# Kernel optimization log

Measured on AMD Instinct MI355X. Metric: run time of the kernel, lower is better.

The kernel has to match this reference:

```python
import jax, jax.numpy as jnp
import numpy as np

H_IMG = 224
W_IMG = 224
CHUNK = 128   # triangles rasterized per scan step
EPS = 1e-8
N_VERTS = 6890
N_FACES = 13776
BATCH = 2


def setup_inputs() -> dict:
    key = jax.random.key(0)
    k0, k1, k2 = jax.random.split(key, 3)
    # vertices in front of the camera (z ~ 2.5) so triangles project into the image
    v = jax.random.normal(k0, (BATCH, N_VERTS, 3), jnp.float32) * 0.3 + jnp.array([0.0, 0.0, 2.5], jnp.float32)
    vc = jax.random.uniform(k1, (N_VERTS, 3), dtype=jnp.float32)          # per-vertex colors
    f = jax.random.randint(k2, (N_FACES, 3), 0, N_VERTS, dtype=jnp.int32)  # triangle list
    bgcolor = jnp.zeros((3,), jnp.float32)
    camera_f = jnp.array([500.0, 500.0], jnp.float32)
    camera_c = jnp.array([112.0, 112.0], jnp.float32)
    camera_t = jnp.zeros((3,), jnp.float32)
    camera_rt = jnp.zeros((3,), jnp.float32)
    return {"v": v, "vc": vc, "bgcolor": bgcolor, "camera_f": camera_f,
            "camera_c": camera_c, "camera_t": camera_t, "camera_rt": camera_rt, "f": f}


def _rodrigues(r):
    # axis-angle -> rotation matrix, safe at r = 0
    th = jnp.sqrt(jnp.sum(r * r) + 1e-12)
    k = r / th
    kx, ky, kz = k[0], k[1], k[2]
    z = jnp.zeros_like(kx)
    K = jnp.stack([jnp.stack([z, -kz, ky]),
                   jnp.stack([kz, z, -kx]),
                   jnp.stack([-ky, kx, z])])
    c, s = jnp.cos(th), jnp.sin(th)
    return c * jnp.eye(3, dtype=r.dtype) + (1.0 - c) * jnp.outer(k, k) + s * K


def _edge(ax, ay, bx, by, px, py):
    # signed area of (a, b, p) * 2
    return (bx - ax) * (py - ay) - (by - ay) * (px - ax)


def _rasterize(uv, zc, vc, faces, bgcolor, height, width):
    """Z-buffered rasterization with perspective-correct barycentric color interp.
    uv: [V,2] screen coords, zc: [V] camera-space depth, vc: [V,C], faces: [F,3]."""
    F, C = faces.shape[0], vc.shape[-1]
    pad = (-F) % CHUNK
    faces_p = jnp.concatenate([faces, jnp.zeros((pad, 3), faces.dtype)], 0)
    fmask = jnp.concatenate([jnp.ones((F,), bool), jnp.zeros((pad,), bool)])
    faces_p = faces_p.reshape(-1, CHUNK, 3)
    fmask = fmask.reshape(-1, CHUNK)

    xs = jnp.arange(width, dtype=jnp.float32) + 0.5
    ys = jnp.arange(height, dtype=jnp.float32) + 0.5
    px, py = jnp.meshgrid(xs, ys)              # [H,W] pixel centers
    cx = px.ravel()[None, :]                    # [1,HW]
    cy = py.ravel()[None, :]
    HW = height * width
    ar = jnp.arange(HW)

    def step(carry, inp):
        zbuf, col = carry
        fc, fm = inp                            # [K,3] int, [K] bool
        p = uv[fc]                              # [K,3,2]
        zt = zc[fc]                             # [K,3]
        x0, y0 = p[:, 0, 0:1], p[:, 0, 1:2]
        x1, y1 = p[:, 1, 0:1], p[:, 1, 1:2]
        x2, y2 = p[:, 2, 0:1], p[:, 2, 1:2]
        w0 = _edge(x1, y1, x2, y2, cx, cy)      # [K,HW]
        w1 = _edge(x2, y2, x0, y0, cx, cy)
        w2 = _edge(x0, y0, x1, y1, cx, cy)
        area = _edge(x0, y0, x1, y1, x2, y2)    # [K,1]
        nz = jnp.abs(area) > EPS
        inv_area = jnp.where(nz, 1.0 / jnp.where(nz, area, 1.0), 0.0)
        b0, b1, b2 = w0 * inv_area, w1 * inv_area, w2 * inv_area
        inside = (b0 >= 0) & (b1 >= 0) & (b2 >= 0)
        zvalid = jnp.all(zt > EPS, axis=1, keepdims=True)
        valid = inside & zvalid & nz & fm[:, None]
        zt_s = jnp.maximum(zt, EPS)
        inv_z = b0 / zt_s[:, 0:1] + b1 / zt_s[:, 1:2] + b2 / zt_s[:, 2:3]
        zp = jnp.where(valid & (inv_z > EPS), 1.0 / jnp.maximum(inv_z, EPS), jnp.inf)
        idx = jnp.argmin(zp, axis=0)            # nearest triangle per pixel in chunk
        zmin = zp[idx, ar]                      # [HW]
        hit = jnp.isfinite(zmin)
        zmin_s = jnp.where(hit, zmin, 1.0)
        bb = jnp.stack([b0, b1, b2], -1)[idx, ar]   # [HW,3]
        fsel = fc[idx]                          # [HW,3]
        zsel = jnp.maximum(zt[idx], EPS)        # [HW,3]
        csel = vc[fsel]                         # [HW,3,C]
        pc = bb / zsel                          # perspective-correct weights / z
        newcol = jnp.einsum('pk,pkc->pc', pc, csel) * zmin_s[:, None]
        upd = hit & (zmin < zbuf)
        zbuf = jnp.where(upd, zmin_s, zbuf)
        col = jnp.where(upd[:, None], newcol, col)
        return (zbuf, col), None

    zbuf0 = jnp.full((HW,), jnp.inf, jnp.float32)
    col0 = jnp.broadcast_to(bgcolor.astype(jnp.float32), (HW, C))
    (zbuf, col), _ = jax.lax.scan(step, (zbuf0, col0), (faces_p, fmask))
    return col.reshape(height, width, C)


def reference(v, vc, bgcolor, camera_f, camera_c, camera_t, camera_rt, f):
    R = _rodrigues(camera_rt)
    vcam = jnp.einsum('bvj,ij->bvi', v, R) + camera_t   # [B,V,3]
    z = vcam[..., 2]
    zs = jnp.maximum(z, EPS)
    uv = vcam[..., :2] / zs[..., None] * camera_f + camera_c  # pinhole projection
    render = jax.vmap(lambda uv_b, z_b: _rasterize(uv_b, z_b, vc, f, bgcolor, H_IMG, W_IMG))
    return render(uv, z)                                   # [B,H,W,C]
```

## Files before the change

kernel.cpp:

```cpp
#include <hip/hip_runtime.h>
#include <math.h>

#define H_IMG 224
#define W_IMG 224
#define HW (H_IMG * W_IMG)
#define EPSF 1e-8f
#define NV 6890
#define NF 13776
#define NB 2
#define FCHUNK 128
#define NCHUNK ((NF + FCHUNK - 1) / FCHUNK)
#define FPAD (NCHUNK * FCHUNK)
#define NWAVE 8
#define NBUCK 1024
#define CHDR_STRIDE 128
#define KEY_INIT 0x7F800000FFFFFFFFULL

#define OFF_ZBU   0u
#define OFF_ZBS   110336u
#define OFF_BBS   220928u
#define OFF_GMS   663296u
#define OFF_OIS   2432768u
#define OFF_INV   2543360u
#define OFF_CHDR  2653696u
#define OFF_CNT   2654720u
#define OFF_OFFS  2662912u

__device__ inline unsigned long long shfl_xor_u64(unsigned long long v, int m) {
  unsigned lo = (unsigned)v, hi = (unsigned)(v >> 32);
  lo = __shfl_xor(lo, m);
  hi = __shfl_xor(hi, m);
  return ((unsigned long long)hi << 32) | lo;
}

struct Cam { float m[9]; float t0, t1, t2, fx, fy, cx, cy; };

__device__ inline Cam load_cam(const float* cf, const float* cc,
                               const float* ct, const float* crt) {
  Cam C;
  float r0 = crt[0], r1 = crt[1], r2 = crt[2];
  float ss = __fadd_rn(__fadd_rn(__fmul_rn(r0, r0), __fmul_rn(r1, r1)), __fmul_rn(r2, r2));
  float th = sqrtf(__fadd_rn(ss, 1e-12f));
  float kx = r0 / th, ky = r1 / th, kz = r2 / th;
  float c = cosf(th), s = sinf(th), oc = 1.0f - c;
  C.m[0] = c + oc * kx * kx;      C.m[1] = oc * kx * ky - s * kz; C.m[2] = oc * kx * kz + s * ky;
  C.m[3] = oc * ky * kx + s * kz; C.m[4] = c + oc * ky * ky;      C.m[5] = oc * ky * kz - s * kx;
  C.m[6] = oc * kz * kx - s * ky; C.m[7] = oc * kz * ky + s * kx; C.m[8] = c + oc * kz * kz;
  C.t0 = ct[0]; C.t1 = ct[1]; C.t2 = ct[2];
  C.fx = cf[0]; C.fy = cf[1]; C.cx = cc[0]; C.cy = cc[1];
  return C;
}

__device__ inline float3 proj_one(const Cam& C, const float* vp) {
  float x = vp[0], y = vp[1], z = vp[2];
  float xc = C.m[0] * x + C.m[1] * y + C.m[2] * z + C.t0;
  float yc = C.m[3] * x + C.m[4] * y + C.m[5] * z + C.t1;
  float zc = C.m[6] * x + C.m[7] * y + C.m[8] * z + C.t2;
  float zs = fmaxf(zc, EPSF);
  float u = __fadd_rn(__fmul_rn(xc / zs, C.fx), C.cx);
  float w = __fadd_rn(__fmul_rn(yc / zs, C.fy), C.cy);
  return make_float3(u, w, zc);
}

__global__ void zb_init_kernel(const float* __restrict__ v, const int* __restrict__ f,
                               const float* __restrict__ cf, const float* __restrict__ cc,
                               const float* __restrict__ ct, const float* __restrict__ crt,
                               float* __restrict__ zbU, unsigned* __restrict__ cnt,
                               float* __restrict__ zbS, float4* __restrict__ bbS) {
  int i = blockIdx.x * blockDim.x + threadIdx.x;
  if (i < NB * FPAD) {
    zbS[i] = 3e30f;
    bbS[i] = make_float4(1e30f, -1e30f, 1e30f, -1e30f);
  }
  if (i >= NB * NF) return;
  int b = i / NF, fi = i - b * NF;
  Cam C = load_cam(cf, cc, ct, crt);
  int i0 = f[fi * 3 + 0], i1 = f[fi * 3 + 1], i2 = f[fi * 3 + 2];
  float3 p0 = proj_one(C, v + ((size_t)b * NV + i0) * 3);
  float3 p1 = proj_one(C, v + ((size_t)b * NV + i1) * 3);
  float3 p2 = proj_one(C, v + ((size_t)b * NV + i2) * 3);
  float area = __fsub_rn(__fmul_rn(__fsub_rn(p1.x, p0.x), __fsub_rn(p2.y, p0.y)),
                         __fmul_rn(__fsub_rn(p1.y, p0.y), __fsub_rn(p2.x, p0.x)));
  bool nz = fabsf(area) > EPSF;
  bool zv = (p0.z > EPSF) && (p1.z > EPSF) && (p2.z > EPSF);
  bool ok = nz && zv;
  float zb;
  if (!ok) {
    zb = 3e30f;
  } else {
    float minz = fminf(fminf(fmaxf(p0.z, EPSF), fmaxf(p1.z, EPSF)), fmaxf(p2.z, EPSF));
    float M = fmaxf(fmaxf(fmaxf(fabsf(p0.x), fabsf(p0.y)), fmaxf(fabsf(p1.x), fabsf(p1.y))),
                    fmaxf(fabsf(p2.x), fabsf(p2.y)));
    float werr = (2.0f * M) * (M + 256.0f) * 6e-7f;
    bool tight = (3.0f * werr) <= (5e-4f * fabsf(area));
    zb = tight ? __fmul_rn(minz, 0.999f) : 0.0f;
  }
  zbU[i] = zb;
  int bucket = (int)fminf(fmaxf(zb * 256.0f, 0.0f), (float)(NBUCK - 1));
  atomicAdd(&cnt[b * NBUCK + bucket], 1u);
}

__global__ __launch_bounds__(1024) void scan_kernel(const unsigned* __restrict__ cnt,
                                                    unsigned* __restrict__ offs,
                                                    unsigned* __restrict__ chdr) {
  __shared__ unsigned wsum[16];
  __shared__ unsigned ends[NBUCK];
  int t = threadIdx.x, b = blockIdx.x;
  int lane = t & 63, wid = t >> 6;
  unsigned v = cnt[b * NBUCK + t];
  unsigned acc = v;
  #pragma unroll
  for (int d = 1; d < 64; d <<= 1) {
    unsigned n = __shfl_up(acc, d);
    if (lane >= d) acc += n;
  }
  if (lane == 63) wsum[wid] = acc;
  __syncthreads();
  if (t < 16) {
    unsigned wv = wsum[t];
    #pragma unroll
    for (int d = 1; d < 16; d <<= 1) {
      unsigned n = __shfl_up(wv, d, 16);
      if (t >= d) wv += n;
    }
    wsum[t] = wv;
  }
  __syncthreads();
  unsigned base = (wid > 0) ? wsum[wid - 1] : 0u;
  unsigned incl = base + acc;
  offs[b * NBUCK + t] = incl - v;
  ends[t] = incl;
  __syncthreads();
  if (t < NCHUNK) {
    unsigned pos0 = (unsigned)(t * FCHUNK);
    int lo = 0, hi = NBUCK - 1;
    while (lo < hi) {
      int mid = (lo + hi) >> 1;
      if (ends[mid] > pos0) hi = mid; else lo = mid + 1;
    }
    chdr[b * CHDR_STRIDE + t] = __float_as_uint((float)lo * (1.0f / 256.0f));
  }
}

__global__ void scatter_kernel(const float* __restrict__ v, const int* __restrict__ f,
                               const float* __restrict__ cf, const float* __restrict__ cc,
                               const float* __restrict__ ct, const float* __restrict__ crt,
                               const float* __restrict__ zbU, unsigned* __restrict__ offs,
                               float* __restrict__ zbS, float4* __restrict__ bbS,
                               float4* __restrict__ gmS, int* __restrict__ oiS,
                               int* __restrict__ inv) {
  int i = blockIdx.x * blockDim.x + threadIdx.x;
  if (i >= NB * NF) return;
  int b = i / NF, fi = i - b * NF;
  float zb = zbU[i];
  int bucket = (int)fminf(fmaxf(zb * 256.0f, 0.0f), (float)(NBUCK - 1));
  unsigned pos = atomicAdd(&offs[b * NBUCK + bucket], 1u);
  Cam C = load_cam(cf, cc, ct, crt);
  int i0 = f[fi * 3 + 0], i1 = f[fi * 3 + 1], i2 = f[fi * 3 + 2];
  float3 p0 = proj_one(C, v + ((size_t)b * NV + i0) * 3);
  float3 p1 = proj_one(C, v + ((size_t)b * NV + i1) * 3);
  float3 p2 = proj_one(C, v + ((size_t)b * NV + i2) * 3);
  float x0 = p0.x, y0 = p0.y, z0 = p0.z;
  float x1 = p1.x, y1 = p1.y, z1 = p1.z;
  float x2 = p2.x, y2 = p2.y, z2 = p2.z;
  float area = __fsub_rn(__fmul_rn(__fsub_rn(x1, x0), __fsub_rn(y2, y0)),
                         __fmul_rn(__fsub_rn(y1, y0), __fsub_rn(x2, x0)));
  bool nz = fabsf(area) > EPSF;
  float inv_area = nz ? (1.0f / area) : 0.0f;
  bool zv = (z0 > EPSF) && (z1 > EPSF) && (z2 > EPSF);
  bool ok = nz && zv;
  float zz0 = ok ? fmaxf(z0, EPSF) : 1e30f;
  float zz1 = ok ? fmaxf(z1, EPSF) : 1e30f;
  float zz2 = ok ? fmaxf(z2, EPSF) : 1e30f;
  size_t sp_ = (size_t)b * FPAD + pos;
  zbS[sp_] = zb;
  bbS[sp_] = make_float4(fminf(fminf(x0, x1), x2), fmaxf(fmaxf(x0, x1), x2),
                         fminf(fminf(y0, y1), y2), fmaxf(fmaxf(y0, y1), y2));
  gmS[sp_ * 4 + 0] = make_float4(__fsub_rn(x2, x1), __fsub_rn(y2, y1), x1, y1);
  gmS[sp_ * 4 + 1] = make_float4(__fsub_rn(x0, x2), __fsub_rn(y0, y2), x2, y2);
  gmS[sp_ * 4 + 2] = make_float4(__fsub_rn(x1, x0), __fsub_rn(y1, y0), x0, y0);
  gmS[sp_ * 4 + 3] = make_float4(zz0, zz1, zz2, inv_area);
  oiS[sp_] = fi;
  inv[i] = (int)pos;
}

__global__ __launch_bounds__(512) void raster_kernel(
    const unsigned* __restrict__ chdr,
    const float* __restrict__ zbS,
    const float4* __restrict__ bbS,
    const float4* __restrict__ gmS,
    const int* __restrict__ oiS,
    const int* __restrict__ inv,
    const int* __restrict__ f,
    const float* __restrict__ vc,
    const float* __restrict__ bg,
    float* __restrict__ out) {
  __shared__ unsigned hint[NWAVE][16];
  __shared__ unsigned long long fin[NWAVE][16];
  int b = blockIdx.z;
  int w = threadIdx.x >> 6;
  int lane = threadIdx.x & 63;
  int slot = lane & 3;
  int p = lane >> 2;
  int wx = blockIdx.x * 4, wy = blockIdx.y * 4;
  int x = wx + (p & 3), y = wy + (p >> 2);
  float px = (float)x + 0.5f, py = (float)y + 0.5f;
  float tx0 = (float)wx + 0.5f, tx1 = (float)wx + 3.5f;
  float ty0 = (float)wy + 0.5f, ty1 = (float)wy + 3.5f;
  const unsigned* chdrB = chdr + b * CHDR_STRIDE;
  const float*  zbB = zbS + (size_t)b * FPAD;
  const float4* bbB = bbS + (size_t)b * FPAD;
  const float4* gmB = gmS + (size_t)b * FPAD * 4;
  const int*    oiB = oiS + (size_t)b * FPAD;

  if (threadIdx.x < NWAVE * 16) hint[threadIdx.x >> 4][threadIdx.x & 15] = 0x7F800000u;
  __syncthreads();

  unsigned long long bestKey = KEY_INIT;

  for (int c = w; c < NCHUNK; c += NWAVE) {
    unsigned z_ = (unsigned)(bestKey >> 32);
    unsigned zo = __shfl_xor(z_, 1); if (zo < z_) z_ = zo;
    zo = __shfl_xor(z_, 2); if (zo < z_) z_ = zo;
    if (slot == 0) hint[w][p] = z_;
    unsigned bzp = hint[0][p];
    #pragma unroll
    for (int hw_ = 1; hw_ < NWAVE; ++hw_) {
      unsigned hh = hint[hw_][p]; if (hh < bzp) bzp = hh;
    }
    float comb = __uint_as_float(bzp);
    float czb = __uint_as_float(chdrB[c]);
    if (!__any(czb <= comb)) break;
    float combMax = fmaxf(comb, __shfl_xor(comb, 4));
    combMax = fmaxf(combMax, __shfl_xor(combMax, 8));
    combMax = fmaxf(combMax, __shfl_xor(combMax, 16));
    combMax = fmaxf(combMax, __shfl_xor(combMax, 32));
    int base = c * FCHUNK;
    #pragma unroll
    for (int h = 0; h < FCHUNK / 64; ++h) {
      int fbase = base + h * 64;
      float zb_lane = zbB[fbase + lane];
      float4 bb = bbB[fbase + lane];
      bool pass = (zb_lane <= combMax) &&
                  (bb.x <= tx1) && (bb.y >= tx0) &&
                  (bb.z <= ty1) && (bb.w >= ty0);
      unsigned long long m = __ballot(pass);
      unsigned long long mm = m;
      while (mm) {
        int bit = __builtin_ctzll(mm);
        int g = bit & ~3;
        mm &= ~(0xFULL << g);
        if ((m >> (g + slot)) & 1) {
          int fi = fbase + g + slot;
          const float4* gm = &gmB[(size_t)fi * 4];
          float4 q0 = gm[0], q1 = gm[1], q2 = gm[2], q3 = gm[3];
          float w0 = __fsub_rn(__fmul_rn(q0.x, __fsub_rn(py, q0.w)),
                               __fmul_rn(q0.y, __fsub_rn(px, q0.z)));
          float w1 = __fsub_rn(__fmul_rn(q1.x, __fsub_rn(py, q1.w)),
                               __fmul_rn(q1.y, __fsub_rn(px, q1.z)));
          float w2 = __fsub_rn(__fmul_rn(q2.x, __fsub_rn(py, q2.w)),
                               __fmul_rn(q2.y, __fsub_rn(px, q2.z)));
          float b0 = __fmul_rn(w0, q3.w);
          float b1 = __fmul_rn(w1, q3.w);
          float b2 = __fmul_rn(w2, q3.w);
          if (b0 >= 0.0f && b1 >= 0.0f && b2 >= 0.0f) {
            float invz = __fadd_rn(__fadd_rn(b0 / q3.x, b1 / q3.y), b2 / q3.z);
            if (invz > EPSF) {
              float zp = 1.0f / invz;
              unsigned long long key =
                  ((unsigned long long)__float_as_uint(zp) << 32) | (unsigned)oiB[fi];
              if (key < bestKey) bestKey = key;
            }
          }
        }
      }
    }
  }

  unsigned long long o = shfl_xor_u64(bestKey, 1);
  if (o < bestKey) bestKey = o;
  o = shfl_xor_u64(bestKey, 2);
  if (o < bestKey) bestKey = o;
  if (slot == 0) fin[w][p] = bestKey;
  __syncthreads();

  int t = threadIdx.x;
  if (t < 16) {
    unsigned long long key = fin[0][t];
    #pragma unroll
    for (int hw_ = 1; hw_ < NWAVE; ++hw_) {
      unsigned long long kk = fin[hw_][t]; if (kk < key) key = kk;
    }
    int xx = wx + (t & 3), yy = wy + (t >> 2);
    float pxx = (float)xx + 0.5f, pyy = (float)yy + 0.5f;
    float o0, o1, o2;
    if (key != KEY_INIT) {
      int best = (int)(unsigned)(key & 0xFFFFFFFFu);
      float zmin = __uint_as_float((unsigned)(key >> 32));
      int pos = inv[b * NF + best];
      const float4* g = &gmB[(size_t)pos * 4];
      float4 q0 = g[0], q1 = g[1], q2 = g[2], q3 = g[3];
      float w0 = __fsub_rn(__fmul_rn(q0.x, __fsub_rn(pyy, q0.w)),
                           __fmul_rn(q0.y, __fsub_rn(pxx, q0.z)));
      float w1 = __fsub_rn(__fmul_rn(q1.x, __fsub_rn(pyy, q1.w)),
                           __fmul_rn(q1.y, __fsub_rn(pxx, q1.z)));
      float w2 = __fsub_rn(__fmul_rn(q2.x, __fsub_rn(pyy, q2.w)),
                           __fmul_rn(q2.y, __fsub_rn(pxx, q2.z)));
      float b0 = __fmul_rn(w0, q3.w), b1 = __fmul_rn(w1, q3.w), b2 = __fmul_rn(w2, q3.w);
      float pc0 = b0 / q3.x, pc1 = b1 / q3.y, pc2 = b2 / q3.z;
      int i0 = f[best * 3 + 0], i1 = f[best * 3 + 1], i2 = f[best * 3 + 2];
      const float* c0p = vc + (size_t)i0 * 3;
      const float* c1p = vc + (size_t)i1 * 3;
      const float* c2p = vc + (size_t)i2 * 3;
      o0 = __fmul_rn(__fadd_rn(__fadd_rn(__fmul_rn(pc0, c0p[0]), __fmul_rn(pc1, c1p[0])),
                               __fmul_rn(pc2, c2p[0])), zmin);
      o1 = __fmul_rn(__fadd_rn(__fadd_rn(__fmul_rn(pc0, c0p[1]), __fmul_rn(pc1, c1p[1])),
                               __fmul_rn(pc2, c2p[1])), zmin);
      o2 = __fmul_rn(__fadd_rn(__fadd_rn(__fmul_rn(pc0, c0p[2]), __fmul_rn(pc1, c1p[2])),
                               __fmul_rn(pc2, c2p[2])), zmin);
    } else {
      o0 = bg[0]; o1 = bg[1]; o2 = bg[2];
    }
    size_t oo = ((size_t)(b * H_IMG + yy) * W_IMG + xx) * 3;
    out[oo + 0] = o0;
    out[oo + 1] = o1;
    out[oo + 2] = o2;
  }
}

extern "C" void kernel_launch(void* const* d_in, const int* in_sizes, int n_in,
                              void* d_out, int out_size, void* d_ws, size_t ws_size,
                              hipStream_t stream) {
  const float* v   = (const float*)d_in[0];
  const float* vc  = (const float*)d_in[1];
  const float* bg  = (const float*)d_in[2];
  const float* cf  = (const float*)d_in[3];
  const float* cc  = (const float*)d_in[4];
  const float* ct  = (const float*)d_in[5];
  const float* crt = (const float*)d_in[6];
  const int*   f   = (const int*)d_in[7];
  float* out = (float*)d_out;
  char* ws = (char*)d_ws;

  float*    zbU   = (float*)(ws + OFF_ZBU);
  float*    zbS   = (float*)(ws + OFF_ZBS);
  float4*   bbS   = (float4*)(ws + OFF_BBS);
  float4*   gmS   = (float4*)(ws + OFF_GMS);
  int*      oiS   = (int*)(ws + OFF_OIS);
  int*      inv   = (int*)(ws + OFF_INV);
  unsigned* chdr  = (unsigned*)(ws + OFF_CHDR);
  unsigned* cnt   = (unsigned*)(ws + OFF_CNT);
  unsigned* offs  = (unsigned*)(ws + OFF_OFFS);

  hipMemsetAsync(cnt, 0, (size_t)NB * NBUCK * 4, stream);
  hipLaunchKernelGGL(zb_init_kernel, dim3((NB * FPAD + 255) / 256), dim3(256), 0, stream,
                     v, f, cf, cc, ct, crt, zbU, cnt, zbS, bbS);
  hipLaunchKernelGGL(scan_kernel, dim3(NB), dim3(1024), 0, stream, cnt, offs, chdr);
  hipLaunchKernelGGL(scatter_kernel, dim3((NB * NF + 255) / 256), dim3(256), 0, stream,
                     v, f, cf, cc, ct, crt, zbU, offs, zbS, bbS, gmS, oiS, inv);
  hipLaunchKernelGGL(raster_kernel, dim3(W_IMG / 4, H_IMG / 4, NB),
                     dim3(512), 0, stream,
                     chdr, zbS, bbS, gmS, oiS, inv, f, vc, bg, out);
}
```

Before: 339.2 us.

## Fuse preprocessing kernels into one cooperative kernel and halve raster waves per block

Result: no change. 335.6 us (-1.1%).

```diff
diff --git a/kernel.cpp b/kernel.cpp
--- a/kernel.cpp
+++ b/kernel.cpp
@@ -1,5 +1,8 @@
 #include <hip/hip_runtime.h>
+#include <hip/hip_cooperative_groups.h>
 #include <math.h>
+
+namespace cg = cooperative_groups;
 
 #define H_IMG 224
 #define W_IMG 224
@@ -11,7 +14,7 @@
 #define FCHUNK 128
 #define NCHUNK ((NF + FCHUNK - 1) / FCHUNK)
 #define FPAD (NCHUNK * FCHUNK)
-#define NWAVE 8
+#define NWAVE 4
 #define NBUCK 1024
 #define CHDR_STRIDE 128
 #define KEY_INIT 0x7F800000FFFFFFFFULL
@@ -62,129 +65,129 @@
   return make_float3(u, w, zc);
 }
 
-__global__ void zb_init_kernel(const float* __restrict__ v, const int* __restrict__ f,
-                               const float* __restrict__ cf, const float* __restrict__ cc,
-                               const float* __restrict__ ct, const float* __restrict__ crt,
-                               float* __restrict__ zbU, unsigned* __restrict__ cnt,
-                               float* __restrict__ zbS, float4* __restrict__ bbS) {
+__global__ void prep_kernel(const float* __restrict__ v, const int* __restrict__ f,
+                            const float* __restrict__ cf, const float* __restrict__ cc,
+                            const float* __restrict__ ct, const float* __restrict__ crt,
+                            float* __restrict__ zbU, unsigned* __restrict__ cnt,
+                            unsigned* __restrict__ offs, unsigned* __restrict__ chdr,
+                            float* __restrict__ zbS, float4* __restrict__ bbS,
+                            float4* __restrict__ gmS, int* __restrict__ oiS,
+                            int* __restrict__ inv) {
+  cg::grid_group grid = cg::this_grid();
   int i = blockIdx.x * blockDim.x + threadIdx.x;
+
+  if (i < NB * NBUCK) cnt[i] = 0u;
   if (i < NB * FPAD) {
     zbS[i] = 3e30f;
     bbS[i] = make_float4(1e30f, -1e30f, 1e30f, -1e30f);
   }
-  if (i >= NB * NF) return;
-  int b = i / NF, fi = i - b * NF;
-  Cam C = load_cam(cf, cc, ct, crt);
-  int i0 = f[fi * 3 + 0], i1 = f[fi * 3 + 1], i2 = f[fi * 3 + 2];
-  float3 p0 = proj_one(C, v + ((size_t)b * NV + i0) * 3);
-  float3 p1 = proj_one(C, v + ((size_t)b * NV + i1) * 3);
-  float3 p2 = proj_one(C, v + ((size_t)b * NV + i2) * 3);
-  float area = __fsub_rn(__fmul_rn(__fsub_rn(p1.x, p0.x), __fsub_rn(p2.y, p0.y)),
-                         __fmul_rn(__fsub_rn(p1.y, p0.y), __fsub_rn(p2.x, p0.x)));
-  bool nz = fabsf(area) > EPSF;
-  bool zv = (p0.z > EPSF) && (p1.z > EPSF) && (p2.z > EPSF);
-  bool ok = nz && zv;
-  float zb;
-  if (!ok) {
-    zb = 3e30f;
-  } else {
-    float minz = fminf(fminf(fmaxf(p0.z, EPSF), fmaxf(p1.z, EPSF)), fmaxf(p2.z, EPSF));
-    float M = fmaxf(fmaxf(fmaxf(fabsf(p0.x), fabsf(p0.y)), fmaxf(fabsf(p1.x), fabsf(p1.y))),
-                    fmaxf(fabsf(p2.x), fabsf(p2.y)));
-    float werr = (2.0f * M) * (M + 256.0f) * 6e-7f;
-    bool tight = (3.0f * werr) <= (5e-4f * fabsf(area));
-    zb = tight ? __fmul_rn(minz, 0.999f) : 0.0f;
-  }
-  zbU[i] = zb;
-  int bucket = (int)fminf(fmaxf(zb * 256.0f, 0.0f), (float)(NBUCK - 1));
-  atomicAdd(&cnt[b * NBUCK + bucket], 1u);
-}
-
-__global__ __launch_bounds__(1024) void scan_kernel(const unsigned* __restrict__ cnt,
-                                                    unsigned* __restrict__ offs,
-                                                    unsigned* __restrict__ chdr) {
-  __shared__ unsigned wsum[16];
+  grid.sync();
+
+  if (i < NB * NF) {
+    int b = i / NF, fi = i - b * NF;
+    Cam C = load_cam(cf, cc, ct, crt);
+    int i0 = f[fi * 3 + 0], i1 = f[fi * 3 + 1], i2 = f[fi * 3 + 2];
+    float3 p0 = proj_one(C, v + ((size_t)b * NV + i0) * 3);
+    float3 p1 = proj_one(C, v + ((size_t)b * NV + i1) * 3);
+    float3 p2 = proj_one(C, v + ((size_t)b * NV + i2) * 3);
+    float area = __fsub_rn(__fmul_rn(__fsub_rn(p1.x, p0.x), __fsub_rn(p2.y, p0.y)),
+                           __fmul_rn(__fsub_rn(p1.y, p0.y), __fsub_rn(p2.x, p0.x)));
+    bool nz = fabsf(area) > EPSF;
+    bool zv = (p0.z > EPSF) && (p1.z > EPSF) && (p2.z > EPSF);
+    bool ok = nz && zv;
+    float zb;
+    if (!ok) {
+      zb = 3e30f;
+    } else {
+      float minz = fminf(fminf(fmaxf(p0.z, EPSF), fmaxf(p1.z, EPSF)), fmaxf(p2.z, EPSF));
+      float M = fmaxf(fmaxf(fmaxf(fabsf(p0.x), fabsf(p0.y)), fmaxf(fabsf(p1.x), fabsf(p1.y))),
+                      fmaxf(fabsf(p2.x), fabsf(p2.y)));
+      float werr = (2.0f * M) * (M + 256.0f) * 6e-7f;
+      bool tight = (3.0f * werr) <= (5e-4f * fabsf(area));
+      zb = tight ? __fmul_rn(minz, 0.999f) : 0.0f;
+    }
+    zbU[i] = zb;
+    int bucket = (int)fminf(fmaxf(zb * 256.0f, 0.0f), (float)(NBUCK - 1));
+    atomicAdd(&cnt[b * NBUCK + bucket], 1u);
+  }
+  grid.sync();
+
   __shared__ unsigned ends[NBUCK];
-  int t = threadIdx.x, b = blockIdx.x;
-  int lane = t & 63, wid = t >> 6;
-  unsigned v = cnt[b * NBUCK + t];
-  unsigned acc = v;
-  #pragma unroll
-  for (int d = 1; d < 64; d <<= 1) {
-    unsigned n = __shfl_up(acc, d);
-    if (lane >= d) acc += n;
-  }
-  if (lane == 63) wsum[wid] = acc;
-  __syncthreads();
-  if (t < 16) {
-    unsigned wv = wsum[t];
-    #pragma unroll
-    for (int d = 1; d < 16; d <<= 1) {
-      unsigned n = __shfl_up(wv, d, 16);
-      if (t >= d) wv += n;
-    }
-    wsum[t] = wv;
-  }
-  __syncthreads();
-  unsigned base = (wid > 0) ? wsum[wid - 1] : 0u;
-  unsigned incl = base + acc;
-  offs[b * NBUCK + t] = incl - v;
-  ends[t] = incl;
-  __syncthreads();
-  if (t < NCHUNK) {
-    unsigned pos0 = (unsigned)(t * FCHUNK);
-    int lo = 0, hi = NBUCK - 1;
-    while (lo < hi) {
-      int mid = (lo + hi) >> 1;
-      if (ends[mid] > pos0) hi = mid; else lo = mid + 1;
-    }
-    chdr[b * CHDR_STRIDE + t] = __float_as_uint((float)lo * (1.0f / 256.0f));
-  }
-}
-
-__global__ void scatter_kernel(const float* __restrict__ v, const int* __restrict__ f,
-                               const float* __restrict__ cf, const float* __restrict__ cc,
-                               const float* __restrict__ ct, const float* __restrict__ crt,
-                               const float* __restrict__ zbU, unsigned* __restrict__ offs,
-                               float* __restrict__ zbS, float4* __restrict__ bbS,
-                               float4* __restrict__ gmS, int* __restrict__ oiS,
-                               int* __restrict__ inv) {
-  int i = blockIdx.x * blockDim.x + threadIdx.x;
-  if (i >= NB * NF) return;
-  int b = i / NF, fi = i - b * NF;
-  float zb = zbU[i];
-  int bucket = (int)fminf(fmaxf(zb * 256.0f, 0.0f), (float)(NBUCK - 1));
-  unsigned pos = atomicAdd(&offs[b * NBUCK + bucket], 1u);
-  Cam C = load_cam(cf, cc, ct, crt);
-  int i0 = f[fi * 3 + 0], i1 = f[fi * 3 + 1], i2 = f[fi * 3 + 2];
-  float3 p0 = proj_one(C, v + ((size_t)b * NV + i0) * 3);
-  float3 p1 = proj_one(C, v + ((size_t)b * NV + i1) * 3);
-  float3 p2 = proj_one(C, v + ((size_t)b * NV + i2) * 3);
-  float x0 = p0.x, y0 = p0.y, z0 = p0.z;
-  float x1 = p1.x, y1 = p1.y, z1 = p1.z;
-  float x2 = p2.x, y2 = p2.y, z2 = p2.z;
-  float area = __fsub_rn(__fmul_rn(__fsub_rn(x1, x0), __fsub_rn(y2, y0)),
-                         __fmul_rn(__fsub_rn(y1, y0), __fsub_rn(x2, x0)));
-  bool nz = fabsf(area) > EPSF;
-  float inv_area = nz ? (1.0f / area) : 0.0f;
-  bool zv = (z0 > EPSF) && (z1 > EPSF) && (z2 > EPSF);
-  bool ok = nz && zv;
-  float zz0 = ok ? fmaxf(z0, EPSF) : 1e30f;
-  float zz1 = ok ? fmaxf(z1, EPSF) : 1e30f;
-  float zz2 = ok ? fmaxf(z2, EPSF) : 1e30f;
-  size_t sp_ = (size_t)b * FPAD + pos;
-  zbS[sp_] = zb;
-  bbS[sp_] = make_float4(fminf(fminf(x0, x1), x2), fmaxf(fmaxf(x0, x1), x2),
-                         fminf(fminf(y0, y1), y2), fmaxf(fmaxf(y0, y1), y2));
-  gmS[sp_ * 4 + 0] = make_float4(__fsub_rn(x2, x1), __fsub_rn(y2, y1), x1, y1);
-  gmS[sp_ * 4 + 1] = make_float4(__fsub_rn(x0, x2), __fsub_rn(y0, y2), x2, y2);
-  gmS[sp_ * 4 + 2] = make_float4(__fsub_rn(x1, x0), __fsub_rn(y1, y0), x0, y0);
-  gmS[sp_ * 4 + 3] = make_float4(zz0, zz1, zz2, inv_area);
-  oiS[sp_] = fi;
-  inv[i] = (int)pos;
-}
-
-__global__ __launch_bounds__(512) void raster_kernel(
+  __shared__ unsigned wsum[4];
+  __shared__ unsigned carry_s;
+  if (blockIdx.x < NB) {
+    int b = blockIdx.x, t = threadIdx.x;
+    int lane = t & 63, wid = t >> 6;
+    if (t == 0) carry_s = 0u;
+    for (int seg = 0; seg < NBUCK / 256; ++seg) {
+      __syncthreads();
+      unsigned carry = carry_s;
+      int idx = seg * 256 + t;
+      unsigned vv = cnt[b * NBUCK + idx];
+      unsigned acc = vv;
+      #pragma unroll
+      for (int d = 1; d < 64; d <<= 1) {
+        unsigned n = __shfl_up(acc, d);
+        if (lane >= d) acc += n;
+      }
+      if (lane == 63) wsum[wid] = acc;
+      __syncthreads();
+      unsigned wbase = 0;
+      for (int k = 0; k < wid; ++k) wbase += wsum[k];
+      unsigned incl = carry + wbase + acc;
+      offs[b * NBUCK + idx] = incl - vv;
+      ends[idx] = incl;
+      if (t == 255) carry_s = incl;
+    }
+    __syncthreads();
+    if (t < NCHUNK) {
+      unsigned pos0 = (unsigned)(t * FCHUNK);
+      int lo = 0, hi = NBUCK - 1;
+      while (lo < hi) {
+        int mid = (lo + hi) >> 1;
+        if (ends[mid] > pos0) hi = mid; else lo = mid + 1;
+      }
+      chdr[b * CHDR_STRIDE + t] = __float_as_uint((float)lo * (1.0f / 256.0f));
+    }
+  }
+  grid.sync();
+
+  if (i < NB * NF) {
+    int b = i / NF, fi = i - b * NF;
+    float zb = zbU[i];
+    int bucket = (int)fminf(fmaxf(zb * 256.0f, 0.0f), (float)(NBUCK - 1));
+    unsigned pos = atomicAdd(&offs[b * NBUCK + bucket], 1u);
+    Cam C = load_cam(cf, cc, ct, crt);
+    int i0 = f[fi * 3 + 0], i1 = f[fi * 3 + 1], i2 = f[fi * 3 + 2];
+    float3 p0 = proj_one(C, v + ((size_t)b * NV + i0) * 3);
+    float3 p1 = proj_one(C, v + ((size_t)b * NV + i1) * 3);
+    float3 p2 = proj_one(C, v + ((size_t)b * NV + i2) * 3);
+    float x0 = p0.x, y0 = p0.y, z0 = p0.z;
+    float x1 = p1.x, y1 = p1.y, z1 = p1.z;
+    float x2 = p2.x, y2 = p2.y, z2 = p2.z;
+    float area = __fsub_rn(__fmul_rn(__fsub_rn(x1, x0), __fsub_rn(y2, y0)),
+                           __fmul_rn(__fsub_rn(y1, y0), __fsub_rn(x2, x0)));
+    bool nz = fabsf(area) > EPSF;
+    float inv_area = nz ? (1.0f / area) : 0.0f;
+    bool zv = (z0 > EPSF) && (z1 > EPSF) && (z2 > EPSF);
+    bool ok = nz && zv;
+    float zz0 = ok ? fmaxf(z0, EPSF) : 1e30f;
+    float zz1 = ok ? fmaxf(z1, EPSF) : 1e30f;
+    float zz2 = ok ? fmaxf(z2, EPSF) : 1e30f;
+    size_t sp_ = (size_t)b * FPAD + pos;
+    zbS[sp_] = zb;
+    bbS[sp_] = make_float4(fminf(fminf(x0, x1), x2), fmaxf(fmaxf(x0, x1), x2),
+                           fminf(fminf(y0, y1), y2), fmaxf(fmaxf(y0, y1), y2));
+    gmS[sp_ * 4 + 0] = make_float4(__fsub_rn(x2, x1), __fsub_rn(y2, y1), x1, y1);
+    gmS[sp_ * 4 + 1] = make_float4(__fsub_rn(x0, x2), __fsub_rn(y0, y2), x2, y2);
+    gmS[sp_ * 4 + 2] = make_float4(__fsub_rn(x1, x0), __fsub_rn(y1, y0), x0, y0);
+    gmS[sp_ * 4 + 3] = make_float4(zz0, zz1, zz2, inv_area);
+    oiS[sp_] = fi;
+    inv[i] = (int)pos;
+  }
+}
+
+__global__ __launch_bounds__(256) void raster_kernel(
     const unsigned* __restrict__ chdr,
     const float* __restrict__ zbS,
     const float4* __restrict__ bbS,
@@ -352,13 +355,14 @@
   unsigned* cnt   = (unsigned*)(ws + OFF_CNT);
   unsigned* offs  = (unsigned*)(ws + OFF_OFFS);
 
-  hipMemsetAsync(cnt, 0, (size_t)NB * NBUCK * 4, stream);
-  hipLaunchKernelGGL(zb_init_kernel, dim3((NB * FPAD + 255) / 256), dim3(256), 0, stream,
-                     v, f, cf, cc, ct, crt, zbU, cnt, zbS, bbS);
-  hipLaunchKernelGGL(scan_kernel, dim3(NB), dim3(1024), 0, stream, cnt, offs, chdr);
-  hipLaunchKernelGGL(scatter_kernel, dim3((NB * NF + 255) / 256), dim3(256), 0, stream,
-                     v, f, cf, cc, ct, crt, zbU, offs, zbS, bbS, gmS, oiS, inv);
+  void* args[] = { (void*)&v, (void*)&f, (void*)&cf, (void*)&cc, (void*)&ct,
+                   (void*)&crt, (void*)&zbU, (void*)&cnt, (void*)&offs,
+                   (void*)&chdr, (void*)&zbS, (void*)&bbS, (void*)&gmS,
+                   (void*)&oiS, (void*)&inv };
+  hipLaunchCooperativeKernel((void*)prep_kernel,
+                             dim3((NB * FPAD + 255) / 256), dim3(256),
+                             args, 0, stream);
   hipLaunchKernelGGL(raster_kernel, dim3(W_IMG / 4, H_IMG / 4, NB),
-                     dim3(512), 0, stream,
+                     dim3(256), 0, stream,
                      chdr, zbS, bbS, gmS, oiS, inv, f, vc, bg, out);
 }
```
